# Performance work log

Hardware: AMD Instinct MI355X
Metric: run time of the kernel (lower is better)

The kernel has to match this reference:

```python
import jax, jax.numpy as jnp
import numpy as np

MEL_W = 1.0
GATE_W = 1.0
ATT_W = 0.1
GA_W = 0.1
SIGMA = 0.4


def setup_inputs() -> dict:
    key = jax.random.key(0)
    ks = jax.random.split(key, 8)
    B, M, T_OUT, T_IN = 64, 80, 2000, 400
    mel_out = jax.random.normal(ks[0], (B, M, T_OUT), dtype=jnp.float32)
    mel_out_postnet = jax.random.normal(ks[1], (B, M, T_OUT), dtype=jnp.float32)
    gate_out = jax.random.normal(ks[2], (B, T_OUT), dtype=jnp.float32)
    align = jax.random.uniform(ks[3], (B, T_OUT, T_IN), dtype=jnp.float32)
    alignments = align / jnp.sum(align, axis=-1, keepdims=True)  # attention-like rows
    mel_target = jax.random.normal(ks[4], (B, M, T_OUT), dtype=jnp.float32)
    gate_target = jax.random.uniform(ks[5], (B, T_OUT), dtype=jnp.float32)
    input_lengths = jax.random.randint(ks[6], (B,), T_IN // 2, T_IN + 1, dtype=jnp.int32)
    output_lengths = jax.random.randint(ks[7], (B,), T_OUT // 2, T_OUT + 1, dtype=jnp.int32)
    return {
        "mel_out": mel_out,
        "mel_out_postnet": mel_out_postnet,
        "gate_out": gate_out,
        "alignments": alignments,
        "mel_target": mel_target,
        "gate_target": gate_target,
        "input_lengths": input_lengths,
        "output_lengths": output_lengths,
    }


def _bce_with_logits(logits, targets):
    # mean of: max(x,0) - x*z + log(1 + exp(-|x|))  (numerically stable)
    return jnp.mean(jnp.maximum(logits, 0.0) - logits * targets
                    + jnp.log1p(jnp.exp(-jnp.abs(logits))))


def reference(mel_out, mel_out_postnet, gate_out, alignments,
              mel_target, gate_target, input_lengths, output_lengths):
    B, T_out, T_in = alignments.shape

    # Mel L1 loss (decoder + postnet)
    mel_loss = (jnp.mean(jnp.abs(mel_out - mel_target))
                + jnp.mean(jnp.abs(mel_out_postnet - mel_target)))

    # Gate BCE-with-logits
    gate_loss = _bce_with_logits(gate_out, gate_target)

    # Monotonic attention penalty: sum of attention strictly below the diagonal
    ii = jnp.arange(T_out)[:, None]   # [T_out, 1]
    jj = jnp.arange(T_in)[None, :]    # [1, T_in]
    backward_mask = (jj < ii).astype(alignments.dtype)  # 1 - triu(ones, 0)
    att_loss = jnp.sum(alignments * backward_mask[None]) / B

    # Guided attention: Gaussian anti-diagonal mask, zero outside valid lengths
    T_in_b = input_lengths.astype(jnp.float32)[:, None, None]    # [B,1,1]
    T_out_b = output_lengths.astype(jnp.float32)[:, None, None]  # [B,1,1]
    i_f = jnp.arange(T_out, dtype=jnp.float32)[None, :, None]    # [1,T_out,1]
    j_f = jnp.arange(T_in, dtype=jnp.float32)[None, None, :]     # [1,1,T_in]
    expected_j = j_f / T_in_b * T_out_b
    w = 1.0 - jnp.exp(-(i_f - expected_j) ** 2 / (2.0 * SIGMA ** 2))
    valid = (jnp.arange(T_out)[None, :, None] < output_lengths[:, None, None]) & \
            (jnp.arange(T_in)[None, None, :] < input_lengths[:, None, None])
    guided = jnp.where(valid, w, 0.0)  # [B, T_out, T_in]
    ga_loss = jnp.sum(alignments * guided) / B

    total = (MEL_W * mel_loss + GATE_W * gate_loss
             + ATT_W * att_loss + GA_W * ga_loss)
    return (total, mel_loss, gate_loss, att_loss, ga_loss)
```

## Files before the change

### kernel.cpp

```cpp
#include <hip/hip_runtime.h>
#include <math.h>

constexpr int Bsz   = 64;
constexpr int Mmel  = 80;
constexpr int Tout  = 2000;
constexpr int Tin   = 400;
constexpr int MEL_N  = Bsz * Mmel * Tout;
constexpr int GATE_N = Bsz * Tout;
constexpr int ALN_N  = Bsz * Tout * Tin;

constexpr float ATT_W = 0.1f;
constexpr float GA_W  = 0.1f;
constexpr float INV_2SIG2 = 3.125f;

constexpr int NBLK = 1024;
constexpr int NTHR = 256;

__device__ __forceinline__ float wave_reduce(float v) {
    #pragma unroll
    for (int off = 32; off > 0; off >>= 1)
        v += __shfl_down(v, off, 64);
    return v;
}

__global__ __launch_bounds__(NTHR) void loss_main(
    const float* __restrict__ mel_out,
    const float* __restrict__ mel_post,
    const float* __restrict__ gate_out,
    const float* __restrict__ align,
    const float* __restrict__ mel_tgt,
    const float* __restrict__ gate_tgt,
    const int*   __restrict__ in_len,
    const int*   __restrict__ out_len,
    double* __restrict__ acc)
{
    const int tid      = blockIdx.x * blockDim.x + threadIdx.x;
    const int nthreads = gridDim.x * blockDim.x;

    float mel_s = 0.f, gate_s = 0.f, att_s = 0.f, ga_s = 0.f;

    {
        const float4* a4 = (const float4*)mel_out;
        const float4* p4 = (const float4*)mel_post;
        const float4* t4 = (const float4*)mel_tgt;
        const int n4 = MEL_N / 4;
        for (int i = tid; i < n4; i += nthreads) {
            float4 a = a4[i], p = p4[i], t = t4[i];
            mel_s += fabsf(a.x - t.x) + fabsf(a.y - t.y) + fabsf(a.z - t.z) + fabsf(a.w - t.w);
            mel_s += fabsf(p.x - t.x) + fabsf(p.y - t.y) + fabsf(p.z - t.z) + fabsf(p.w - t.w);
        }
    }

    {
        const float4* x4 = (const float4*)gate_out;
        const float4* z4 = (const float4*)gate_tgt;
        const int n4 = GATE_N / 4;
        for (int i = tid; i < n4; i += nthreads) {
            float4 x = x4[i], z = z4[i];
            gate_s += fmaxf(x.x, 0.f) - x.x * z.x + log1pf(expf(-fabsf(x.x)));
            gate_s += fmaxf(x.y, 0.f) - x.y * z.y + log1pf(expf(-fabsf(x.y)));
            gate_s += fmaxf(x.z, 0.f) - x.z * z.z + log1pf(expf(-fabsf(x.z)));
            gate_s += fmaxf(x.w, 0.f) - x.w * z.w + log1pf(expf(-fabsf(x.w)));
        }
    }

    {
        const float4* al4 = (const float4*)align;
        const int n4 = ALN_N / 4;
        constexpr int TIN4 = Tin / 4;
        for (int i = tid; i < n4; i += nthreads) {
            float4 a = al4[i];
            const int row  = i / TIN4;
            const int j0   = (i - row * TIN4) * 4;
            const int irow = row % Tout;
            const int b    = row / Tout;
            const int il   = in_len[b];
            const int ol   = out_len[b];
            const float scale = (float)ol / (float)il;
            const bool row_valid = irow < ol;
            const float fi = (float)irow;

            const float av[4] = {a.x, a.y, a.z, a.w};
            #pragma unroll
            for (int k = 0; k < 4; ++k) {
                const int jj = j0 + k;
                if (jj < irow) att_s += av[k];
                if (row_valid && jj < il) {
                    const float d = fi - (float)jj * scale;
                    ga_s += av[k] * (1.0f - __expf(-d * d * INV_2SIG2));
                }
            }
        }
    }

    __shared__ float smem[4][4];
    const int lane = threadIdx.x & 63;
    const int wid  = threadIdx.x >> 6;

    mel_s  = wave_reduce(mel_s);
    gate_s = wave_reduce(gate_s);
    att_s  = wave_reduce(att_s);
    ga_s   = wave_reduce(ga_s);
    if (lane == 0) {
        smem[wid][0] = mel_s;
        smem[wid][1] = gate_s;
        smem[wid][2] = att_s;
        smem[wid][3] = ga_s;
    }
    __syncthreads();
    if (threadIdx.x == 0) {
        float m = 0.f, g = 0.f, at = 0.f, ga = 0.f;
        #pragma unroll
        for (int w = 0; w < NTHR / 64; ++w) {
            m  += smem[w][0];
            g  += smem[w][1];
            at += smem[w][2];
            ga += smem[w][3];
        }
        atomicAdd(&acc[0], (double)m);
        atomicAdd(&acc[1], (double)g);
        atomicAdd(&acc[2], (double)at);
        atomicAdd(&acc[3], (double)ga);
    }
}

__global__ void loss_final(const double* __restrict__ acc, float* __restrict__ out) {
    const double mel  = acc[0] / (double)MEL_N;
    const double gate = acc[1] / (double)GATE_N;
    const double att  = acc[2] / (double)Bsz;
    const double ga   = acc[3] / (double)Bsz;
    const double total = mel + gate + (double)ATT_W * att + (double)GA_W * ga;
    out[0] = (float)total;
    out[1] = (float)mel;
    out[2] = (float)gate;
    out[3] = (float)att;
    out[4] = (float)ga;
}

extern "C" void kernel_launch(void* const* d_in, const int* in_sizes, int n_in,
                              void* d_out, int out_size, void* d_ws, size_t ws_size,
                              hipStream_t stream) {
    const float* mel_out  = (const float*)d_in[0];
    const float* mel_post = (const float*)d_in[1];
    const float* gate_out = (const float*)d_in[2];
    const float* align    = (const float*)d_in[3];
    const float* mel_tgt  = (const float*)d_in[4];
    const float* gate_tgt = (const float*)d_in[5];
    const int*   in_len   = (const int*)d_in[6];
    const int*   out_len  = (const int*)d_in[7];

    double* acc = (double*)d_ws;
    hipMemsetAsync(acc, 0, 4 * sizeof(double), stream);

    loss_main<<<NBLK, NTHR, 0, stream>>>(mel_out, mel_post, gate_out, align,
                                         mel_tgt, gate_tgt, in_len, out_len, acc);
    loss_final<<<1, 1, 0, stream>>>(acc, (float*)d_out);
}
```

Baseline: 404.7 us.

## Raise grid size, unroll loads, cache lengths in LDS, replace atomics with partials

The grid grows from 1024 to 6144 blocks, and the streaming loops are unrolled two ways (mel) and four ways (alignments) so each thread has more loads in flight. Per-batch lengths and scale factors move into shared memory, and the branchy guided-attention math becomes branch-free selects. Double atomics and the memset are replaced by per-block float4 partials, reduced by a 512-thread final kernel. The branch-free form computes exp for masked elements too, and per-block partials are summed in float before the double reduction.

```diff
diff --git a/kernel.cpp b/kernel.cpp
--- a/kernel.cpp
+++ b/kernel.cpp
@@ -8,12 +8,13 @@
 constexpr int MEL_N  = Bsz * Mmel * Tout;
 constexpr int GATE_N = Bsz * Tout;
 constexpr int ALN_N  = Bsz * Tout * Tin;
+constexpr int TIN4   = Tin / 4;
 
 constexpr float ATT_W = 0.1f;
 constexpr float GA_W  = 0.1f;
 constexpr float INV_2SIG2 = 3.125f;
 
-constexpr int NBLK = 1024;
+constexpr int NBLK = 6144;
 constexpr int NTHR = 256;
 
 __device__ __forceinline__ float wave_reduce(float v) {
@@ -21,6 +22,40 @@
     for (int off = 32; off > 0; off >>= 1)
         v += __shfl_down(v, off, 64);
     return v;
+}
+
+__device__ __forceinline__ double wave_reduce_d(double v) {
+    #pragma unroll
+    for (int off = 32; off > 0; off >>= 1)
+        v += __shfl_down(v, off, 64);
+    return v;
+}
+
+__device__ __forceinline__ void process_aln(
+    float4 a, int i,
+    const int* __restrict__ s_il, const int* __restrict__ s_ol,
+    const float* __restrict__ s_scale,
+    float& att_s, float& ga_s)
+{
+    const int row  = i / TIN4;
+    const int j0   = (i - row * TIN4) * 4;
+    const int irow = row % Tout;
+    const int b    = row / Tout;
+    const int il   = s_il[b];
+    const int ol   = s_ol[b];
+    const float scale = s_scale[b];
+    const bool row_valid = irow < ol;
+    const float fi = (float)irow;
+
+    const float av[4] = {a.x, a.y, a.z, a.w};
+    #pragma unroll
+    for (int k = 0; k < 4; ++k) {
+        const int jj = j0 + k;
+        att_s += (jj < irow) ? av[k] : 0.0f;
+        const float d = fi - (float)jj * scale;
+        const float w = 1.0f - __expf(-d * d * INV_2SIG2);
+        ga_s += (row_valid && jj < il) ? av[k] * w : 0.0f;
+    }
 }
 
 __global__ __launch_bounds__(NTHR) void loss_main(
@@ -32,10 +67,22 @@
     const float* __restrict__ gate_tgt,
     const int*   __restrict__ in_len,
     const int*   __restrict__ out_len,
-    double* __restrict__ acc)
+    float4* __restrict__ partials)
 {
-    const int tid      = blockIdx.x * blockDim.x + threadIdx.x;
-    const int nthreads = gridDim.x * blockDim.x;
+    __shared__ int   s_il[Bsz];
+    __shared__ int   s_ol[Bsz];
+    __shared__ float s_scale[Bsz];
+    if (threadIdx.x < Bsz) {
+        const int il = in_len[threadIdx.x];
+        const int ol = out_len[threadIdx.x];
+        s_il[threadIdx.x] = il;
+        s_ol[threadIdx.x] = ol;
+        s_scale[threadIdx.x] = (float)ol / (float)il;
+    }
+    __syncthreads();
+
+    const int tid    = blockIdx.x * blockDim.x + threadIdx.x;
+    const int stride = gridDim.x * blockDim.x;
 
     float mel_s = 0.f, gate_s = 0.f, att_s = 0.f, ga_s = 0.f;
 
@@ -44,7 +91,18 @@
         const float4* p4 = (const float4*)mel_post;
         const float4* t4 = (const float4*)mel_tgt;
         const int n4 = MEL_N / 4;
-        for (int i = tid; i < n4; i += nthreads) {
+        int i = tid;
+        for (; i + stride < n4; i += 2 * stride) {
+            const int i1 = i + stride;
+            float4 a0 = a4[i],  a1 = a4[i1];
+            float4 p0 = p4[i],  p1 = p4[i1];
+            float4 t0 = t4[i],  t1 = t4[i1];
+            mel_s += fabsf(a0.x - t0.x) + fabsf(a0.y - t0.y) + fabsf(a0.z - t0.z) + fabsf(a0.w - t0.w);
+            mel_s += fabsf(p0.x - t0.x) + fabsf(p0.y - t0.y) + fabsf(p0.z - t0.z) + fabsf(p0.w - t0.w);
+            mel_s += fabsf(a1.x - t1.x) + fabsf(a1.y - t1.y) + fabsf(a1.z - t1.z) + fabsf(a1.w - t1.w);
+            mel_s += fabsf(p1.x - t1.x) + fabsf(p1.y - t1.y) + fabsf(p1.z - t1.z) + fabsf(p1.w - t1.w);
+        }
+        for (; i < n4; i += stride) {
             float4 a = a4[i], p = p4[i], t = t4[i];
             mel_s += fabsf(a.x - t.x) + fabsf(a.y - t.y) + fabsf(a.z - t.z) + fabsf(a.w - t.w);
             mel_s += fabsf(p.x - t.x) + fabsf(p.y - t.y) + fabsf(p.z - t.z) + fabsf(p.w - t.w);
@@ -55,7 +113,7 @@
         const float4* x4 = (const float4*)gate_out;
         const float4* z4 = (const float4*)gate_tgt;
         const int n4 = GATE_N / 4;
-        for (int i = tid; i < n4; i += nthreads) {
+        for (int i = tid; i < n4; i += stride) {
             float4 x = x4[i], z = z4[i];
             gate_s += fmaxf(x.x, 0.f) - x.x * z.x + log1pf(expf(-fabsf(x.x)));
             gate_s += fmaxf(x.y, 0.f) - x.y * z.y + log1pf(expf(-fabsf(x.y)));
@@ -67,33 +125,22 @@
     {
         const float4* al4 = (const float4*)align;
         const int n4 = ALN_N / 4;
-        constexpr int TIN4 = Tin / 4;
-        for (int i = tid; i < n4; i += nthreads) {
-            float4 a = al4[i];
-            const int row  = i / TIN4;
-            const int j0   = (i - row * TIN4) * 4;
-            const int irow = row % Tout;
-            const int b    = row / Tout;
-            const int il   = in_len[b];
-            const int ol   = out_len[b];
-            const float scale = (float)ol / (float)il;
-            const bool row_valid = irow < ol;
-            const float fi = (float)irow;
-
-            const float av[4] = {a.x, a.y, a.z, a.w};
-            #pragma unroll
-            for (int k = 0; k < 4; ++k) {
-                const int jj = j0 + k;
-                if (jj < irow) att_s += av[k];
-                if (row_valid && jj < il) {
-                    const float d = fi - (float)jj * scale;
-                    ga_s += av[k] * (1.0f - __expf(-d * d * INV_2SIG2));
-                }
-            }
-        }
-    }
-
-    __shared__ float smem[4][4];
+        int i = tid;
+        for (; i + 3 * stride < n4; i += 4 * stride) {
+            float4 a0 = al4[i];
+            float4 a1 = al4[i + stride];
+            float4 a2 = al4[i + 2 * stride];
+            float4 a3 = al4[i + 3 * stride];
+            process_aln(a0, i,              s_il, s_ol, s_scale, att_s, ga_s);
+            process_aln(a1, i + stride,     s_il, s_ol, s_scale, att_s, ga_s);
+            process_aln(a2, i + 2 * stride, s_il, s_ol, s_scale, att_s, ga_s);
+            process_aln(a3, i + 3 * stride, s_il, s_ol, s_scale, att_s, ga_s);
+        }
+        for (; i < n4; i += stride)
+            process_aln(al4[i], i, s_il, s_ol, s_scale, att_s, ga_s);
+    }
+
+    __shared__ float smem[NTHR / 64][4];
     const int lane = threadIdx.x & 63;
     const int wid  = threadIdx.x >> 6;
 
@@ -117,24 +164,47 @@
             at += smem[w][2];
             ga += smem[w][3];
         }
-        atomicAdd(&acc[0], (double)m);
-        atomicAdd(&acc[1], (double)g);
-        atomicAdd(&acc[2], (double)at);
-        atomicAdd(&acc[3], (double)ga);
-    }
-}
-
-__global__ void loss_final(const double* __restrict__ acc, float* __restrict__ out) {
-    const double mel  = acc[0] / (double)MEL_N;
-    const double gate = acc[1] / (double)GATE_N;
-    const double att  = acc[2] / (double)Bsz;
-    const double ga   = acc[3] / (double)Bsz;
-    const double total = mel + gate + (double)ATT_W * att + (double)GA_W * ga;
-    out[0] = (float)total;
-    out[1] = (float)mel;
-    out[2] = (float)gate;
-    out[3] = (float)att;
-    out[4] = (float)ga;
+        partials[blockIdx.x] = make_float4(m, g, at, ga);
+    }
+}
+
+__global__ __launch_bounds__(512) void loss_final(
+    const float4* __restrict__ partials, float* __restrict__ out)
+{
+    double m = 0.0, g = 0.0, at = 0.0, ga = 0.0;
+    for (int i = threadIdx.x; i < NBLK; i += 512) {
+        float4 p = partials[i];
+        m += p.x; g += p.y; at += p.z; ga += p.w;
+    }
+    m  = wave_reduce_d(m);
+    g  = wave_reduce_d(g);
+    at = wave_reduce_d(at);
+    ga = wave_reduce_d(ga);
+
+    __shared__ double smem[8][4];
+    const int lane = threadIdx.x & 63;
+    const int wid  = threadIdx.x >> 6;
+    if (lane == 0) {
+        smem[wid][0] = m; smem[wid][1] = g; smem[wid][2] = at; smem[wid][3] = ga;
+    }
+    __syncthreads();
+    if (threadIdx.x == 0) {
+        double ms = 0, gs = 0, ats = 0, gas = 0;
+        #pragma unroll
+        for (int w = 0; w < 8; ++w) {
+            ms += smem[w][0]; gs += smem[w][1]; ats += smem[w][2]; gas += smem[w][3];
+        }
+        const double mel  = ms  / (double)MEL_N;
+        const double gate = gs  / (double)GATE_N;
+        const double att  = ats / (double)Bsz;
+        const double gav  = gas / (double)Bsz;
+        const double total = mel + gate + (double)ATT_W * att + (double)GA_W * gav;
+        out[0] = (float)total;
+        out[1] = (float)mel;
+        out[2] = (float)gate;
+        out[3] = (float)att;
+        out[4] = (float)gav;
+    }
 }
 
 extern "C" void kernel_launch(void* const* d_in, const int* in_sizes, int n_in,
@@ -149,10 +219,9 @@
     const int*   in_len   = (const int*)d_in[6];
     const int*   out_len  = (const int*)d_in[7];
 
-    double* acc = (double*)d_ws;
-    hipMemsetAsync(acc, 0, 4 * sizeof(double), stream);
+    float4* partials = (float4*)d_ws;
 
     loss_main<<<NBLK, NTHR, 0, stream>>>(mel_out, mel_post, gate_out, align,
-                                         mel_tgt, gate_tgt, in_len, out_len, acc);
-    loss_final<<<1, 1, 0, stream>>>(acc, (float*)d_out);
-}
+                                         mel_tgt, gate_tgt, in_len, out_len, partials);
+    loss_final<<<1, 512, 0, stream>>>(partials, (float*)d_out);
+}
```

After: 372.7 us. 7.9% less time.
